# Kernel optimization log

Measured on AMD Instinct MI355X. Metric: run time of the kernel, lower is better.

The kernel has to match this reference:

```python
import jax, jax.numpy as jnp
import numpy as np

# Config constants (mirroring repo globals C.*)
B, L, D = 128, 200, 256          # batch, history length, d_model
NT = 10000                        # num_types (items)
NU = 50000                        # C.USER_NUMBER
NL = 4                            # n_layers
BETA_1 = 0.1                      # C.BETA_1


def _l2norm(x, eps):
    n = jnp.linalg.norm(x, axis=-1, keepdims=True)
    return x / jnp.maximum(n, eps)


def setup_inputs() -> dict:
    key = jax.random.key(0)
    ks = jax.random.split(key, 7)
    user_id = jax.random.randint(ks[0], (B,), 1, NU)
    event_type = jax.random.randint(ks[1], (B, L), 1, NT + 1)  # 1..NT (non-pad)
    adjacent_matrix = jax.random.uniform(ks[2], (NT, NT), jnp.float32)
    pop_encoding = jax.random.normal(ks[3], (NT + 1, D), jnp.float32) * 0.02
    event_emb_w = (jax.random.normal(ks[4], (NT + 1, D), jnp.float32) * 0.02).at[0].set(0.0)
    user_emb_w = (jax.random.normal(ks[5], (NU, D), jnp.float32) * 0.02).at[0].set(0.0)
    layer_ws = jax.random.normal(ks[6], (NL, D, D), jnp.float32) * 0.05
    return {"user_id": user_id, "event_type": event_type,
            "adjacent_matrix": adjacent_matrix, "pop_encoding": pop_encoding,
            "event_emb_w": event_emb_w, "user_emb_w": user_emb_w,
            "layer_ws": layer_ws}


def reference(user_id, event_type, adjacent_matrix, pop_encoding,
              event_emb_w, user_emb_w, layer_ws):
    # non-pad mask (pad idx = 0)
    non_pad = (event_type != 0).astype(jnp.float32)[..., None]  # (B,L,1)

    enc = event_emb_w[event_type]                 # (B,L,D)
    user = user_emb_w[user_id]                    # (B,D)
    pop = pop_encoding[event_type] * non_pad      # (B,L,D)

    # user-specific disentanglement: enc += sign(enc) * normalize(user)
    enc = enc + jnp.sign(enc) * _l2norm(user, 1e-12)[:, None, :]

    # batched adjacency gather: adj[b] = A[e-1][:, e-1] + A[e-1, e-1] (row-broadcast)
    idx = event_type - 1                          # (B,L)
    adj = adjacent_matrix[idx[:, :, None], idx[:, None, :]]      # (B,L,L)
    adj = adj + adjacent_matrix[idx, idx][:, None, :]            # diag broadcast over rows

    # hGCN layer stack: x <- leaky_relu((adj @ x) @ W)
    for i in range(NL):
        enc = jax.nn.leaky_relu(jnp.einsum('bls,bsd->bld', adj, enc) @ layer_ws[i])

    output = enc.mean(axis=1)                     # (B,D)
    user_embeddings = jnp.concatenate([output, pop.mean(axis=1) * BETA_1], axis=-1)  # (B,2D)

    # Predictor (evaluation=True path)
    item_encoding = event_emb_w[1:]               # (NT,D)
    out = user_embeddings[:, :D] @ item_encoding.T  # (B,NT)
    out = _l2norm(out, 1e-5)
    prediction = jnp.tanh(out)
    return prediction, user_embeddings, pop
```

## Files before the change

### kernel.cpp

```cpp
#include <hip/hip_runtime.h>
#include <math.h>

#define B_ 128
#define L_ 200
#define D_ 256
#define NT_ 10000
#define NL_ 4
#define BETA1 0.1f

typedef _Float16 f16x8 __attribute__((ext_vector_type(8)));
typedef _Float16 f16x4 __attribute__((ext_vector_type(4)));
typedef _Float16 f16x2 __attribute__((ext_vector_type(2)));
typedef float f32x4 __attribute__((ext_vector_type(4)));

__device__ __forceinline__ void split2(float v, _Float16& h, _Float16& l) {
    h = (_Float16)v;
    l = (_Float16)(v - (float)h);
}

struct HL { _Float16 h, l; };
__device__ __forceinline__ HL split2v(float v) {
    HL r;
    r.h = (_Float16)v;
    r.l = (_Float16)(v - (float)r.h);
    return r;
}

__device__ __forceinline__ float getscale(const unsigned int* amax, int i, int extra) {
    float am = fmaxf(__uint_as_float(amax[i]), 1e-30f);
    return scalbnf(1.f, 6 - ilogbf(am) - extra);
}

__global__ void init_kernel(float* __restrict__ ue, float* __restrict__ uePred,
                            unsigned int* __restrict__ amax) {
    int bid = blockIdx.x, tid = threadIdx.x;
    if (bid < 512) ue[bid * 256 + tid] = 0.f;
    else if (bid < 640) uePred[(bid - 512) * 256 + tid] = 0.f;
    else if (tid < 16) amax[tid] = 0u;
}

__global__ void user_norm_kernel(const int* __restrict__ user_id,
                                 const float* __restrict__ user_emb_w,
                                 float* __restrict__ unorm) {
    int b = blockIdx.x;
    int d = threadIdx.x;
    int uid = user_id[b];
    float v = user_emb_w[(long)uid * D_ + d];
    float sq = v * v;
    for (int off = 32; off > 0; off >>= 1) sq += __shfl_down(sq, off, 64);
    __shared__ float s[4];
    int wid = d >> 6, lane = d & 63;
    if (lane == 0) s[wid] = sq;
    __syncthreads();
    float n = sqrtf(s[0] + s[1] + s[2] + s[3]);
    n = fmaxf(n, 1e-12f);
    unorm[b * D_ + d] = v / n;
}

__global__ void enc0_kernel(const int* __restrict__ event_type,
                            const float* __restrict__ E,
                            const float* __restrict__ unorm,
                            float* __restrict__ encF,
                            unsigned int* __restrict__ amax) {
    int d = threadIdx.x;
    float m = 0.f;
    for (int bl = blockIdx.x; bl < B_ * L_; bl += gridDim.x) {
        int b = bl / L_;
        int et = event_type[bl];
        float e = E[(long)et * D_ + d];
        float sg = (e > 0.f) ? 1.f : ((e < 0.f) ? -1.f : 0.f);
        float u = unorm[b * D_ + d];
        float v = e + sg * u;
        encF[(long)bl * D_ + d] = v;
        m = fmaxf(m, fabsf(v));
    }
    for (int off = 32; off > 0; off >>= 1) m = fmaxf(m, __shfl_down(m, off, 64));
    __shared__ float sm[4];
    int wid = d >> 6, lane = d & 63;
    if (lane == 0) sm[wid] = m;
    __syncthreads();
    if (d == 0)
        atomicMax(amax, __float_as_uint(fmaxf(fmaxf(sm[0], sm[1]), fmaxf(sm[2], sm[3]))));
}

__global__ void pop_kernel(const int* __restrict__ event_type,
                           const float* __restrict__ pope,
                           float* __restrict__ pop_out) {
    int bl = blockIdx.x;
    int d = threadIdx.x;
    int et = event_type[bl];
    float np = (et != 0) ? 1.0f : 0.0f;
    pop_out[(long)bl * D_ + d] = pope[(long)et * D_ + d] * np;
}

__global__ void diag_kernel(const int* __restrict__ event_type,
                            const float* __restrict__ A,
                            float* __restrict__ diag) {
    int i = blockIdx.x * blockDim.x + threadIdx.x;
    if (i >= B_ * L_) return;
    long idx = (long)event_type[i] - 1;
    diag[i] = A[idx * NT_ + idx];
}

__global__ void adj_split_kernel(const int* __restrict__ event_type,
                                 const float* __restrict__ A,
                                 const float* __restrict__ diag,
                                 _Float16* __restrict__ adjH,
                                 _Float16* __restrict__ adjL) {
    int b = blockIdx.y;
    int i = blockIdx.x;
    int j = threadIdx.x;
    __shared__ int sidx[L_];
    __shared__ float sdiag[L_];
    if (j < L_) {
        sidx[j]  = event_type[b * L_ + j] - 1;
        sdiag[j] = diag[b * L_ + j];
    }
    __syncthreads();
    if (j >= L_) return;
    long row = (long)event_type[b * L_ + i] - 1;
    float v = A[row * NT_ + sidx[j]] + sdiag[j];
    long o = ((long)b * L_ + i) * L_ + j;
    _Float16 h, l;
    split2(v, h, l);
    adjH[o] = h; adjL[o] = l;
}

__global__ void wsplit_kernel(const float* __restrict__ W,
                              _Float16* __restrict__ WTh,
                              _Float16* __restrict__ WTl) {
    int layer = blockIdx.z;
    int k0 = blockIdx.y * 64, n0 = blockIdx.x * 64;
    const float* Wl = W + (long)layer * D_ * D_;
    __shared__ float t[64][65];
    int tid = threadIdx.x;
    for (int i = 0; i < 16; i++) {
        int idx = i * 256 + tid;
        int k = idx >> 6, n = idx & 63;
        t[k][n] = Wl[(long)(k0 + k) * D_ + n0 + n];
    }
    __syncthreads();
    for (int i = 0; i < 16; i++) {
        int idx = i * 256 + tid;
        int n = idx >> 6, k = idx & 63;
        float v = t[k][n];
        long o = (long)layer * D_ * D_ + (long)(n0 + n) * D_ + (k0 + k);
        _Float16 h, l;
        split2(v, h, l);
        WTh[o] = h; WTl[o] = l;
    }
}

__global__ void esplit_kernel(const float* __restrict__ E,
                              _Float16* __restrict__ ETh,
                              _Float16* __restrict__ ETl) {
    long f = ((long)blockIdx.x * 256 + threadIdx.x) * 4;
    float4 v = *(const float4*)(E + D_ + f);
    f16x4 h, l;
    HL r0 = split2v(v.x); h[0] = r0.h; l[0] = r0.l;
    HL r1 = split2v(v.y); h[1] = r1.h; l[1] = r1.l;
    HL r2 = split2v(v.z); h[2] = r2.h; l[2] = r2.l;
    HL r3 = split2v(v.w); h[3] = r3.h; l[3] = r3.l;
    *(f16x4*)(ETh + f) = h;
    *(f16x4*)(ETl + f) = l;
}

__global__ __launch_bounds__(256) void gemm1_kernel(
    const _Float16* __restrict__ adjH, const _Float16* __restrict__ adjL,
    const float* __restrict__ encF,
    _Float16* __restrict__ tmpH, _Float16* __restrict__ tmpL,
    const unsigned int* __restrict__ amax, int layer) {
    int b = blockIdx.z;
    const _Float16* Ah = adjH + (long)b * L_ * L_;
    const _Float16* Al = adjL + (long)b * L_ * L_;
    const float*    Bf = encF + (long)b * L_ * D_;
    int m0 = blockIdx.y * 128, n0 = blockIdx.x * 128;
    int tid = threadIdx.x, lane = tid & 63, wid = tid >> 6;
    int wr = wid >> 1, wc = wid & 1;
    float scale = getscale(amax, layer, 0);

    __shared__ _Float16 sAh[128][40], sAl[128][40];
    __shared__ _Float16 sBh[128][40], sBl[128][40];

    f32x4 acc[4][4] = {};
    int fr = lane & 15, kb = (lane >> 4) * 8, fq = lane >> 4;
    int nst = tid & 127, kkst = tid >> 7;

    for (int k0 = 0; k0 < L_; k0 += 32) {
#pragma unroll
        for (int c = 0; c < 2; c++) {
            int idx = c * 256 + tid;
            int row = idx >> 2, kq = (idx & 3) * 8;
            int gk = k0 + kq;
            f16x8 vh = {}, vl = {};
            if (m0 + row < L_ && gk < L_) {
                long o = (long)(m0 + row) * L_ + gk;
                vh = *(const f16x8*)(Ah + o);
                vl = *(const f16x8*)(Al + o);
            }
            *(f16x8*)&sAh[row][kq] = vh;
            *(f16x8*)&sAl[row][kq] = vl;
        }
#pragma unroll
        for (int it = 0; it < 8; it++) {
            int k = kkst * 16 + it * 2;
            int gk0 = k0 + k;
            float v0 = (gk0     < L_) ? Bf[(long)gk0 * D_ + n0 + nst] * scale : 0.f;
            float v1 = (gk0 + 1 < L_) ? Bf[(long)(gk0 + 1) * D_ + n0 + nst] * scale : 0.f;
            f16x2 h, l;
            HL r0 = split2v(v0); h[0] = r0.h; l[0] = r0.l;
            HL r1 = split2v(v1); h[1] = r1.h; l[1] = r1.l;
            int kx = k ^ ((nst & 3) << 3);
            *(f16x2*)&sBh[nst][kx] = h;
            *(f16x2*)&sBl[nst][kx] = l;
        }
        __syncthreads();

        f16x8 fbh[4], fbl[4];
#pragma unroll
        for (int n = 0; n < 4; n++) {
            int rB = wc * 64 + n * 16 + fr;
            int kbB = kb ^ ((rB & 3) << 3);
            fbh[n] = *(const f16x8*)&sBh[rB][kbB];
            fbl[n] = *(const f16x8*)&sBl[rB][kbB];
        }
#pragma unroll
        for (int m = 0; m < 4; m++) {
            int rA = wr * 64 + m * 16 + fr;
            f16x8 fah = *(const f16x8*)&sAh[rA][kb];
            f16x8 fal = *(const f16x8*)&sAl[rA][kb];
#pragma unroll
            for (int n = 0; n < 4; n++) {
                acc[m][n] = __builtin_amdgcn_mfma_f32_16x16x32_f16(fah, fbh[n], acc[m][n], 0, 0, 0);
                acc[m][n] = __builtin_amdgcn_mfma_f32_16x16x32_f16(fah, fbl[n], acc[m][n], 0, 0, 0);
                acc[m][n] = __builtin_amdgcn_mfma_f32_16x16x32_f16(fal, fbh[n], acc[m][n], 0, 0, 0);
            }
        }
        __syncthreads();
    }

    _Float16* Ch = tmpH + (long)b * L_ * D_;
    _Float16* Cl = tmpL + (long)b * L_ * D_;
#pragma unroll
    for (int m = 0; m < 4; m++)
#pragma unroll
        for (int n = 0; n < 4; n++)
#pragma unroll
            for (int r = 0; r < 4; r++) {
                int row = m0 + wr * 64 + m * 16 + fq * 4 + r;
                int col = n0 + wc * 64 + n * 16 + fr;
                if (row < L_) {
                    float v = acc[m][n][r];
                    _Float16 h, l;
                    split2(v, h, l);
                    long o = (long)row * D_ + col;
                    Ch[o] = h; Cl[o] = l;
                }
            }
}

__global__ __launch_bounds__(256) void gemm2_kernel(
    const _Float16* __restrict__ Ah, const _Float16* __restrict__ Al,
    const _Float16* __restrict__ Bh, const _Float16* __restrict__ Bl,
    float* __restrict__ Cf, unsigned int* __restrict__ amax) {
    int m0 = blockIdx.y * 128, n0 = blockIdx.x * 128;
    int tid = threadIdx.x, lane = tid & 63, wid = tid >> 6;
    int wr = wid >> 1, wc = wid & 1;
    __shared__ _Float16 sAh[128][40], sAl[128][40];
    __shared__ _Float16 sBh[128][40], sBl[128][40];
    __shared__ float sRed[4];
    f32x4 acc[4][4] = {};
    int fr = lane & 15, kb = (lane >> 4) * 8, fq = lane >> 4;

    for (int k0 = 0; k0 < D_; k0 += 32) {
#pragma unroll
        for (int c = 0; c < 2; c++) {
            int idx = c * 256 + tid;
            int row = idx >> 2, kq = (idx & 3) * 8, gk = k0 + kq;
            long oa = (long)(m0 + row) * D_ + gk;
            *(f16x8*)&sAh[row][kq] = *(const f16x8*)(Ah + oa);
            *(f16x8*)&sAl[row][kq] = *(const f16x8*)(Al + oa);
            long ob = (long)(n0 + row) * D_ + gk;
            *(f16x8*)&sBh[row][kq] = *(const f16x8*)(Bh + ob);
            *(f16x8*)&sBl[row][kq] = *(const f16x8*)(Bl + ob);
        }
        __syncthreads();
        f16x8 fbh[4], fbl[4];
#pragma unroll
        for (int n = 0; n < 4; n++) {
            int rB = wc * 64 + n * 16 + fr;
            fbh[n] = *(const f16x8*)&sBh[rB][kb];
            fbl[n] = *(const f16x8*)&sBl[rB][kb];
        }
#pragma unroll
        for (int m = 0; m < 4; m++) {
            int rA = wr * 64 + m * 16 + fr;
            f16x8 fah = *(const f16x8*)&sAh[rA][kb];
            f16x8 fal = *(const f16x8*)&sAl[rA][kb];
#pragma unroll
            for (int n = 0; n < 4; n++) {
                acc[m][n] = __builtin_amdgcn_mfma_f32_16x16x32_f16(fah, fbh[n], acc[m][n], 0, 0, 0);
                acc[m][n] = __builtin_amdgcn_mfma_f32_16x16x32_f16(fah, fbl[n], acc[m][n], 0, 0, 0);
                acc[m][n] = __builtin_amdgcn_mfma_f32_16x16x32_f16(fal, fbh[n], acc[m][n], 0, 0, 0);
            }
        }
        __syncthreads();
    }

    float tmax = 0.f;
#pragma unroll
    for (int m = 0; m < 4; m++)
#pragma unroll
        for (int n = 0; n < 4; n++)
#pragma unroll
            for (int r = 0; r < 4; r++) {
                int row = m0 + wr * 64 + m * 16 + fq * 4 + r;
                int col = n0 + wc * 64 + n * 16 + fr;
                float v = acc[m][n][r];
                v = (v >= 0.f) ? v : 0.01f * v;
                Cf[(long)row * D_ + col] = v;
                tmax = fmaxf(tmax, fabsf(v));
            }
    for (int off = 32; off > 0; off >>= 1) tmax = fmaxf(tmax, __shfl_down(tmax, off, 64));
    if (lane == 0) sRed[wid] = tmax;
    __syncthreads();
    if (tid == 0)
        atomicMax(amax, __float_as_uint(fmaxf(fmaxf(sRed[0], sRed[1]), fmaxf(sRed[2], sRed[3]))));
}

__global__ void mean_kernel(const float* __restrict__ encF,
                            const int* __restrict__ event_type,
                            const float* __restrict__ pope,
                            const unsigned int* __restrict__ amax,
                            float* __restrict__ ue,
                            float* __restrict__ uePred) {
    int b = blockIdx.x, chunk = blockIdx.y, d = threadIdx.x;
    float S = 1.f;
    for (int i = 0; i < NL_; i++) S *= getscale(amax, i, 0);
    float s1 = 0.f, s2 = 0.f;
    int l0 = chunk * 40;
    for (int l = l0; l < l0 + 40; l++) {
        s1 += encF[((long)b * L_ + l) * D_ + d];
        int et = event_type[b * L_ + l];
        s2 += (et != 0) ? pope[(long)et * D_ + d] : 0.f;
    }
    atomicAdd(&ue[b * 2 * D_ + d], s1 / (float)L_ / S);
    atomicAdd(&ue[b * 2 * D_ + D_ + d], s2 * (BETA1 / (float)L_));
    atomicAdd(&uePred[b * D_ + d], s1);
}

__global__ void uesplit_kernel(const float* __restrict__ uePred,
                               const unsigned int* __restrict__ amax,
                               _Float16* __restrict__ ueh,
                               _Float16* __restrict__ uel) {
    int b = blockIdx.x, d = threadIdx.x;
    float scale = getscale(amax, NL_, 8);
    float v = uePred[b * D_ + d] * scale;
    _Float16 h, l;
    split2(v, h, l);
    ueh[b * D_ + d] = h;
    uel[b * D_ + d] = l;
}

__global__ __launch_bounds__(256) void pred_mfma_kernel(
    const _Float16* __restrict__ Ah, const _Float16* __restrict__ Al,
    const _Float16* __restrict__ Bh, const _Float16* __restrict__ Bl,
    float* __restrict__ Cf) {
    int n0 = blockIdx.x * 64;
    int tid = threadIdx.x, lane = tid & 63, wid = tid >> 6;
    int wr = wid >> 1, wc = wid & 1;
    __shared__ _Float16 sAh[128][40], sAl[128][40];
    __shared__ _Float16 sBh[64][40], sBl[64][40];
    f32x4 acc[4][2] = {};
    int fr = lane & 15, kb = (lane >> 4) * 8, fq = lane >> 4;

    for (int k0 = 0; k0 < D_; k0 += 32) {
#pragma unroll
        for (int c = 0; c < 2; c++) {
            int idx = c * 256 + tid;
            int row = idx >> 2, kq = (idx & 3) * 8, gk = k0 + kq;
            long oa = (long)row * D_ + gk;
            *(f16x8*)&sAh[row][kq] = *(const f16x8*)(Ah + oa);
            *(f16x8*)&sAl[row][kq] = *(const f16x8*)(Al + oa);
        }
        {
            int row = tid >> 2, kq = (tid & 3) * 8, gk = k0 + kq;
            f16x8 wh = {}, wl = {};
            if (n0 + row < NT_) {
                long ob = (long)(n0 + row) * D_ + gk;
                wh = *(const f16x8*)(Bh + ob);
                wl = *(const f16x8*)(Bl + ob);
            }
            *(f16x8*)&sBh[row][kq] = wh;
            *(f16x8*)&sBl[row][kq] = wl;
        }
        __syncthreads();
        f16x8 fbh[2], fbl[2];
#pragma unroll
        for (int n = 0; n < 2; n++) {
            int rB = wc * 32 + n * 16 + fr;
            fbh[n] = *(const f16x8*)&sBh[rB][kb];
            fbl[n] = *(const f16x8*)&sBl[rB][kb];
        }
#pragma unroll
        for (int m = 0; m < 4; m++) {
            int rA = wr * 64 + m * 16 + fr;
            f16x8 fah = *(const f16x8*)&sAh[rA][kb];
            f16x8 fal = *(const f16x8*)&sAl[rA][kb];
#pragma unroll
            for (int n = 0; n < 2; n++) {
                acc[m][n] = __builtin_amdgcn_mfma_f32_16x16x32_f16(fah, fbh[n], acc[m][n], 0, 0, 0);
                acc[m][n] = __builtin_amdgcn_mfma_f32_16x16x32_f16(fah, fbl[n], acc[m][n], 0, 0, 0);
                acc[m][n] = __builtin_amdgcn_mfma_f32_16x16x32_f16(fal, fbh[n], acc[m][n], 0, 0, 0);
            }
        }
        __syncthreads();
    }
#pragma unroll
    for (int m = 0; m < 4; m++)
#pragma unroll
        for (int n = 0; n < 2; n++)
#pragma unroll
            for (int r = 0; r < 4; r++) {
                int row = wr * 64 + m * 16 + fq * 4 + r;
                int col = n0 + wc * 32 + n * 16 + fr;
                if (col < NT_)
                    Cf[(long)row * NT_ + col] = acc[m][n][r];
            }
}

__global__ void norms_kernel(const float* __restrict__ pred, float* __restrict__ norms) {
    int b = blockIdx.x, t = threadIdx.x;
    const float* row = pred + (long)b * NT_;
    float sq = 0.f;
    for (int i = t; i < NT_; i += 1024) { float v = row[i]; sq += v * v; }
    for (int off = 32; off > 0; off >>= 1) sq += __shfl_down(sq, off, 64);
    __shared__ float s[16];
    if ((t & 63) == 0) s[t >> 6] = sq;
    __syncthreads();
    if (t == 0) {
        float n = 0.f;
        for (int i = 0; i < 16; i++) n += s[i];
        norms[b] = 1.f / fmaxf(sqrtf(n), 1e-5f);
    }
}

__global__ void tanh_apply_kernel(float* __restrict__ pred, const float* __restrict__ norms) {
    int b = blockIdx.x, chunk = blockIdx.y, t = threadIdx.x;
    float inv = norms[b];
    float* row = pred + (long)b * NT_;
    int start = chunk * 2000;
    for (int i = start + t; i < start + 2000; i += 256)
        row[i] = tanhf(row[i] * inv);
}

template <bool BT, bool LEAKY>
__global__ void gemm_kernel(const float* __restrict__ A,
                            const float* __restrict__ Bm,
                            float* __restrict__ C,
                            int M, int N, int K, int lda, int ldb, int ldc,
                            long strideA, long strideB, long strideC) {
    int batch = blockIdx.z;
    A  += (long)batch * strideA;
    Bm += (long)batch * strideB;
    C  += (long)batch * strideC;
    const int BM = 64, BN = 64, BK = 16;
    __shared__ float As[BK][BM + 1];
    __shared__ float Bs[BK][BN + 1];
    int tid = threadIdx.x;
    int m0 = blockIdx.y * BM, n0 = blockIdx.x * BN;
    int tx = tid & 15, ty = tid >> 4;
    float acc[4][4] = {};
    for (int k0 = 0; k0 < K; k0 += BK) {
        {
            int m = tid >> 2, kk = (tid & 3) * 4;
            int gm = m0 + m;
#pragma unroll
            for (int q = 0; q < 4; q++) {
                int gk = k0 + kk + q;
                float x = (gm < M && gk < K) ? A[(long)gm * lda + gk] : 0.f;
                As[kk + q][m] = x;
            }
        }
        if (!BT) {
            int kk = tid >> 4, n = (tid & 15) * 4;
            int gk = k0 + kk;
#pragma unroll
            for (int q = 0; q < 4; q++) {
                int gn = n0 + n + q;
                float x = (gk < K && gn < N) ? Bm[(long)gk * ldb + gn] : 0.f;
                Bs[kk][n + q] = x;
            }
        } else {
            int n = tid >> 2, kk = (tid & 3) * 4;
            int gn = n0 + n;
#pragma unroll
            for (int q = 0; q < 4; q++) {
                int gk = k0 + kk + q;
                float x = (gn < N && gk < K) ? Bm[(long)gn * ldb + gk] : 0.f;
                Bs[kk + q][n] = x;
            }
        }
        __syncthreads();
#pragma unroll
        for (int kk = 0; kk < BK; kk++) {
            float a[4], bv[4];
#pragma unroll
            for (int q = 0; q < 4; q++) a[q] = As[kk][ty * 4 + q];
#pragma unroll
            for (int q = 0; q < 4; q++) bv[q] = Bs[kk][tx * 4 + q];
#pragma unroll
            for (int i = 0; i < 4; i++)
#pragma unroll
                for (int j = 0; j < 4; j++)
                    acc[i][j] += a[i] * bv[j];
        }
        __syncthreads();
    }
#pragma unroll
    for (int i = 0; i < 4; i++) {
        int gm = m0 + ty * 4 + i;
        if (gm >= M) continue;
#pragma unroll
        for (int j = 0; j < 4; j++) {
            int gn = n0 + tx * 4 + j;
            if (gn >= N) continue;
            float v = acc[i][j];
            if (LEAKY) v = (v >= 0.f) ? v : 0.01f * v;
            C[(long)gm * ldc + gn] = v;
        }
    }
}

__global__ void mean_plain_kernel(const float* __restrict__ enc,
                                  const int* __restrict__ event_type,
                                  const float* __restrict__ pope,
                                  float* __restrict__ ue) {
    int b = blockIdx.x, d = threadIdx.x;
    float s1 = 0.f, s2 = 0.f;
    for (int l = 0; l < L_; l++) {
        s1 += enc[((long)b * L_ + l) * D_ + d];
        int et = event_type[b * L_ + l];
        float np = (et != 0) ? 1.0f : 0.0f;
        s2 += pope[(long)et * D_ + d] * np;
    }
    ue[b * (2 * D_) + d]      = s1 / (float)L_;
    ue[b * (2 * D_) + D_ + d] = (s2 / (float)L_) * BETA1;
}

__global__ void adj_kernel_f32(const int* __restrict__ event_type,
                               const float* __restrict__ A,
                               const float* __restrict__ diag,
                               float* __restrict__ adj) {
    int b = blockIdx.y;
    int i = blockIdx.x;
    int j = threadIdx.x;
    __shared__ int sidx[L_];
    __shared__ float sdiag[L_];
    if (j < L_) {
        sidx[j]  = event_type[b * L_ + j] - 1;
        sdiag[j] = diag[b * L_ + j];
    }
    __syncthreads();
    if (j >= L_) return;
    long row = (long)event_type[b * L_ + i] - 1;
    adj[((long)b * L_ + i) * L_ + j] = A[row * NT_ + sidx[j]] + sdiag[j];
}

__global__ void normtanh_kernel(float* __restrict__ pred) {
    int b = blockIdx.x;
    int t = threadIdx.x;
    float* row = pred + (long)b * NT_;
    float sq = 0.f;
    for (int i = t; i < NT_; i += 256) { float v = row[i]; sq += v * v; }
    for (int off = 32; off > 0; off >>= 1) sq += __shfl_down(sq, off, 64);
    __shared__ float s[4];
    int wid = t >> 6, lane = t & 63;
    if (lane == 0) s[wid] = sq;
    __syncthreads();
    float n = sqrtf(s[0] + s[1] + s[2] + s[3]);
    n = fmaxf(n, 1e-5f);
    float inv = 1.f / n;
    for (int i = t; i < NT_; i += 256) row[i] = tanhf(row[i] * inv);
}

extern "C" void kernel_launch(void* const* d_in, const int* in_sizes, int n_in,
                              void* d_out, int out_size, void* d_ws, size_t ws_size,
                              hipStream_t stream) {
    const int*   user_id    = (const int*)d_in[0];
    const int*   event_type = (const int*)d_in[1];
    const float* A          = (const float*)d_in[2];
    const float* pope       = (const float*)d_in[3];
    const float* E          = (const float*)d_in[4];
    const float* U          = (const float*)d_in[5];
    const float* W          = (const float*)d_in[6];

    float* out  = (float*)d_out;
    float* pred = out;
    float* ue   = out + (long)B_ * NT_;
    float* pop  = ue  + (long)B_ * 2 * D_;

    char* w = (char*)d_ws;
    auto carve = [&](size_t bytes) { char* p = w; w += (bytes + 255) & ~(size_t)255; return p; };
    unsigned int* amax = (unsigned int*)carve(64);
    _Float16* adjH   = (_Float16*)carve((size_t)B_ * L_ * L_ * 2);
    _Float16* adjL   = (_Float16*)carve((size_t)B_ * L_ * L_ * 2);
    _Float16* tmpH   = (_Float16*)carve((size_t)B_ * L_ * D_ * 2);
    _Float16* tmpL   = (_Float16*)carve((size_t)B_ * L_ * D_ * 2);
    float*    encF   = (float*)carve((size_t)B_ * L_ * D_ * 4);
    _Float16* WTh    = (_Float16*)carve((size_t)NL_ * D_ * D_ * 2);
    _Float16* WTl    = (_Float16*)carve((size_t)NL_ * D_ * D_ * 2);
    _Float16* ETh    = (_Float16*)carve((size_t)NT_ * D_ * 2);
    _Float16* ETl    = (_Float16*)carve((size_t)NT_ * D_ * 2);
    float*    uePred = (float*)carve((size_t)B_ * D_ * 4);
    _Float16* ueh    = (_Float16*)carve((size_t)B_ * D_ * 2);
    _Float16* uel    = (_Float16*)carve((size_t)B_ * D_ * 2);
    float*    unorm  = (float*)carve((size_t)B_ * D_ * 4);
    float*    diag   = (float*)carve((size_t)B_ * L_ * 4);
    float*    norms  = (float*)carve((size_t)B_ * 4);
    size_t needed = (size_t)(w - (char*)d_ws);

    if (ws_size >= needed) {
        init_kernel<<<641, 256, 0, stream>>>(ue, uePred, amax);
        user_norm_kernel<<<B_, 256, 0, stream>>>(user_id, U, unorm);
        enc0_kernel<<<1280, 256, 0, stream>>>(event_type, E, unorm, encF, amax);
        pop_kernel<<<B_ * L_, 256, 0, stream>>>(event_type, pope, pop);
        diag_kernel<<<(B_ * L_ + 255) / 256, 256, 0, stream>>>(event_type, A, diag);
        adj_split_kernel<<<dim3(L_, B_), 256, 0, stream>>>(event_type, A, diag, adjH, adjL);
        wsplit_kernel<<<dim3(4, 4, NL_), 256, 0, stream>>>(W, WTh, WTl);
        esplit_kernel<<<NT_ * D_ / 1024, 256, 0, stream>>>(E, ETh, ETl);

        for (int i = 0; i < NL_; i++) {
            gemm1_kernel<<<dim3(2, 2, B_), 256, 0, stream>>>(
                adjH, adjL, encF, tmpH, tmpL, amax, i);
            gemm2_kernel<<<dim3(2, B_ * L_ / 128), 256, 0, stream>>>(
                tmpH, tmpL, WTh + (long)i * D_ * D_, WTl + (long)i * D_ * D_,
                encF, amax + i + 1);
        }

        mean_kernel<<<dim3(B_, 5), 256, 0, stream>>>(encF, event_type, pope, amax, ue, uePred);
        uesplit_kernel<<<B_, 256, 0, stream>>>(uePred, amax, ueh, uel);
        pred_mfma_kernel<<<(NT_ + 63) / 64, 256, 0, stream>>>(ueh, uel, ETh, ETl, pred);
        norms_kernel<<<B_, 1024, 0, stream>>>(pred, norms);
        tanh_apply_kernel<<<dim3(B_, 5), 256, 0, stream>>>(pred, norms);
    } else {
        float* ws0   = (float*)d_ws;
        float* uno   = ws0;
        float* dia   = uno + B_ * D_;
        float* adjF  = dia + B_ * L_;
        float* encA  = adjF + (long)B_ * L_ * L_;
        float* encB  = encA + (long)B_ * L_ * D_;
        float* tmp   = pop;

        user_norm_kernel<<<B_, 256, 0, stream>>>(user_id, U, uno);
        enc0_kernel<<<1280, 256, 0, stream>>>(event_type, E, uno, encA, (unsigned int*)dia);
        diag_kernel<<<(B_ * L_ + 255) / 256, 256, 0, stream>>>(event_type, A, dia);
        adj_kernel_f32<<<dim3(L_, B_), 256, 0, stream>>>(event_type, A, dia, adjF);

        float* cur = encA; float* nxt = encB;
        for (int i = 0; i < NL_; i++) {
            dim3 g1((D_ + 63) / 64, (L_ + 63) / 64, B_);
            gemm_kernel<false, false><<<g1, 256, 0, stream>>>(
                adjF, cur, tmp, L_, D_, L_, L_, D_, D_,
                (long)L_ * L_, (long)L_ * D_, (long)L_ * D_);
            dim3 g2((D_ + 63) / 64, (B_ * L_ + 63) / 64, 1);
            gemm_kernel<false, true><<<g2, 256, 0, stream>>>(
                tmp, W + (long)i * D_ * D_, nxt, B_ * L_, D_, D_, D_, D_, D_, 0, 0, 0);
            float* t = cur; cur = nxt; nxt = t;
        }
        pop_kernel<<<B_ * L_, 256, 0, stream>>>(event_type, pope, pop);
        mean_plain_kernel<<<B_, 256, 0, stream>>>(cur, event_type, pope, ue);

        dim3 g3((NT_ + 63) / 64, (B_ + 63) / 64, 1);
        gemm_kernel<true, false><<<g3, 256, 0, stream>>>(
            ue, E + D_, pred, B_, NT_, D_, 2 * D_, D_, NT_, 0, 0, 0);
        normtanh_kernel<<<B_, 256, 0, stream>>>(pred);
    }
}
```

Measured before the change: 432.5 us.

## Fuse per-layer GEMM pair, merge enc/pop, mean/split and norm/tanh kernels

Each layer now runs one kernel that computes adj@enc into registers, splits the result to fp16 hi/lo pairs in shared memory, and multiplies it by W in place. This removes the intermediate tmp buffer and one launch per layer. Also merges pop into enc0, mean with uesplit (removing atomics and the init of ue/uePred), and norms with tanh, and batches 25 rows per block in the adjacency gather. In exchange, the fused layer kernel has only 256 blocks of 512 threads and large shared memory, which lowers occupancy. It also reads W fragments straight from global memory.

```diff
diff --git a/kernel.cpp b/kernel.cpp
--- a/kernel.cpp
+++ b/kernel.cpp
@@ -31,12 +31,8 @@
     return scalbnf(1.f, 6 - ilogbf(am) - extra);
 }
 
-__global__ void init_kernel(float* __restrict__ ue, float* __restrict__ uePred,
-                            unsigned int* __restrict__ amax) {
-    int bid = blockIdx.x, tid = threadIdx.x;
-    if (bid < 512) ue[bid * 256 + tid] = 0.f;
-    else if (bid < 640) uePred[(bid - 512) * 256 + tid] = 0.f;
-    else if (tid < 16) amax[tid] = 0u;
+__global__ void init_amax_kernel(unsigned int* __restrict__ amax) {
+    if (threadIdx.x < 16) amax[threadIdx.x] = 0u;
 }
 
 __global__ void user_norm_kernel(const int* __restrict__ user_id,
@@ -57,11 +53,13 @@
     unorm[b * D_ + d] = v / n;
 }
 
-__global__ void enc0_kernel(const int* __restrict__ event_type,
-                            const float* __restrict__ E,
-                            const float* __restrict__ unorm,
-                            float* __restrict__ encF,
-                            unsigned int* __restrict__ amax) {
+__global__ void enc0pop_kernel(const int* __restrict__ event_type,
+                               const float* __restrict__ E,
+                               const float* __restrict__ pope,
+                               const float* __restrict__ unorm,
+                               float* __restrict__ encF,
+                               float* __restrict__ pop_out,
+                               unsigned int* __restrict__ amax) {
     int d = threadIdx.x;
     float m = 0.f;
     for (int bl = blockIdx.x; bl < B_ * L_; bl += gridDim.x) {
@@ -73,6 +71,7 @@
         float v = e + sg * u;
         encF[(long)bl * D_ + d] = v;
         m = fmaxf(m, fabsf(v));
+        pop_out[(long)bl * D_ + d] = (et != 0) ? pope[(long)et * D_ + d] : 0.f;
     }
     for (int off = 32; off > 0; off >>= 1) m = fmaxf(m, __shfl_down(m, off, 64));
     __shared__ float sm[4];
@@ -81,16 +80,6 @@
     __syncthreads();
     if (d == 0)
         atomicMax(amax, __float_as_uint(fmaxf(fmaxf(sm[0], sm[1]), fmaxf(sm[2], sm[3]))));
-}
-
-__global__ void pop_kernel(const int* __restrict__ event_type,
-                           const float* __restrict__ pope,
-                           float* __restrict__ pop_out) {
-    int bl = blockIdx.x;
-    int d = threadIdx.x;
-    int et = event_type[bl];
-    float np = (et != 0) ? 1.0f : 0.0f;
-    pop_out[(long)bl * D_ + d] = pope[(long)et * D_ + d] * np;
 }
 
 __global__ void diag_kernel(const int* __restrict__ event_type,
@@ -102,13 +91,13 @@
     diag[i] = A[idx * NT_ + idx];
 }
 
-__global__ void adj_split_kernel(const int* __restrict__ event_type,
-                                 const float* __restrict__ A,
-                                 const float* __restrict__ diag,
-                                 _Float16* __restrict__ adjH,
-                                 _Float16* __restrict__ adjL) {
+__global__ void adj_split2_kernel(const int* __restrict__ event_type,
+                                  const float* __restrict__ A,
+                                  const float* __restrict__ diag,
+                                  _Float16* __restrict__ adjH,
+                                  _Float16* __restrict__ adjL) {
     int b = blockIdx.y;
-    int i = blockIdx.x;
+    int chunk = blockIdx.x;
     int j = threadIdx.x;
     __shared__ int sidx[L_];
     __shared__ float sdiag[L_];
@@ -118,12 +107,15 @@
     }
     __syncthreads();
     if (j >= L_) return;
-    long row = (long)event_type[b * L_ + i] - 1;
-    float v = A[row * NT_ + sidx[j]] + sdiag[j];
-    long o = ((long)b * L_ + i) * L_ + j;
-    _Float16 h, l;
-    split2(v, h, l);
-    adjH[o] = h; adjL[o] = l;
+    int i0 = chunk * 25;
+#pragma unroll 5
+    for (int i = i0; i < i0 + 25; i++) {
+        long rowi = (long)sidx[i];
+        float v = A[rowi * NT_ + sidx[j]] + sdiag[j];
+        HL r = split2v(v);
+        long o = ((long)b * L_ + i) * L_ + j;
+        adjH[o] = r.h; adjL[o] = r.l;
+    }
 }
 
 __global__ void wsplit_kernel(const float* __restrict__ W,
@@ -165,33 +157,37 @@
     *(f16x4*)(ETl + f) = l;
 }
 
-__global__ __launch_bounds__(256) void gemm1_kernel(
-    const _Float16* __restrict__ adjH, const _Float16* __restrict__ adjL,
-    const float* __restrict__ encF,
-    _Float16* __restrict__ tmpH, _Float16* __restrict__ tmpL,
-    const unsigned int* __restrict__ amax, int layer) {
-    int b = blockIdx.z;
-    const _Float16* Ah = adjH + (long)b * L_ * L_;
-    const _Float16* Al = adjL + (long)b * L_ * L_;
-    const float*    Bf = encF + (long)b * L_ * D_;
-    int m0 = blockIdx.y * 128, n0 = blockIdx.x * 128;
+__global__ __launch_bounds__(512) void layer_fused_kernel(
+    const _Float16* __restrict__ adjHg, const _Float16* __restrict__ adjLg,
+    const float* __restrict__ encIn,
+    const _Float16* __restrict__ WThg, const _Float16* __restrict__ WTlg,
+    float* __restrict__ encOut,
+    const unsigned int* __restrict__ amaxIn, unsigned int* __restrict__ amaxOut) {
+    int b = blockIdx.y;
+    int m0 = blockIdx.x * 128;
+    const _Float16* Ah = adjHg + (long)b * L_ * L_;
+    const _Float16* Al = adjLg + (long)b * L_ * L_;
+    const float*    Bf = encIn + (long)b * L_ * D_;
     int tid = threadIdx.x, lane = tid & 63, wid = tid >> 6;
-    int wr = wid >> 1, wc = wid & 1;
-    float scale = getscale(amax, layer, 0);
-
-    __shared__ _Float16 sAh[128][40], sAl[128][40];
-    __shared__ _Float16 sBh[128][40], sBl[128][40];
-
-    f32x4 acc[4][4] = {};
-    int fr = lane & 15, kb = (lane >> 4) * 8, fq = lane >> 4;
-    int nst = tid & 127, kkst = tid >> 7;
+    int wr = wid >> 2, wc = wid & 3;
+    int fr = lane & 15, fq = lane >> 4, kb = fq * 8;
+    float scale = getscale(amaxIn, 0, 0);
+
+    __shared__ char smem[61440];
+    __shared__ float sRed[8];
+    _Float16 (*sAh)[40] = (_Float16(*)[40])(smem);
+    _Float16 (*sAl)[40] = (_Float16(*)[40])(smem + 10240);
+    _Float16 (*sBh)[40] = (_Float16(*)[40])(smem + 20480);
+    _Float16 (*sBl)[40] = (_Float16(*)[40])(smem + 40960);
+    _Float16 (*tH)[80]  = (_Float16(*)[80])(smem + 20480);
+    _Float16 (*tL)[80]  = (_Float16(*)[80])(smem + 40960);
+
+    f32x4 acc1[4][4] = {};
+    int nst = tid & 255, kst = tid >> 8;
 
     for (int k0 = 0; k0 < L_; k0 += 32) {
-#pragma unroll
-        for (int c = 0; c < 2; c++) {
-            int idx = c * 256 + tid;
-            int row = idx >> 2, kq = (idx & 3) * 8;
-            int gk = k0 + kq;
+        {
+            int row = tid >> 2, kq = (tid & 3) * 8, gk = k0 + kq;
             f16x8 vh = {}, vl = {};
             if (m0 + row < L_ && gk < L_) {
                 long o = (long)(m0 + row) * L_ + gk;
@@ -203,10 +199,10 @@
         }
 #pragma unroll
         for (int it = 0; it < 8; it++) {
-            int k = kkst * 16 + it * 2;
+            int k = kst * 16 + it * 2;
             int gk0 = k0 + k;
-            float v0 = (gk0     < L_) ? Bf[(long)gk0 * D_ + n0 + nst] * scale : 0.f;
-            float v1 = (gk0 + 1 < L_) ? Bf[(long)(gk0 + 1) * D_ + n0 + nst] * scale : 0.f;
+            float v0 = (gk0     < L_) ? Bf[(long)gk0 * D_ + nst] * scale : 0.f;
+            float v1 = (gk0 + 1 < L_) ? Bf[(long)(gk0 + 1) * D_ + nst] * scale : 0.f;
             f16x2 h, l;
             HL r0 = split2v(v0); h[0] = r0.h; l[0] = r0.l;
             HL r1 = split2v(v1); h[1] = r1.h; l[1] = r1.l;
@@ -220,9 +216,9 @@
 #pragma unroll
         for (int n = 0; n < 4; n++) {
             int rB = wc * 64 + n * 16 + fr;
-            int kbB = kb ^ ((rB & 3) << 3);
-            fbh[n] = *(const f16x8*)&sBh[rB][kbB];
-            fbl[n] = *(const f16x8*)&sBl[rB][kbB];
+            int kx = kb ^ ((rB & 3) << 3);
+            fbh[n] = *(const f16x8*)&sBh[rB][kx];
+            fbl[n] = *(const f16x8*)&sBl[rB][kx];
         }
 #pragma unroll
         for (int m = 0; m < 4; m++) {
@@ -231,16 +227,61 @@
             f16x8 fal = *(const f16x8*)&sAl[rA][kb];
 #pragma unroll
             for (int n = 0; n < 4; n++) {
-                acc[m][n] = __builtin_amdgcn_mfma_f32_16x16x32_f16(fah, fbh[n], acc[m][n], 0, 0, 0);
-                acc[m][n] = __builtin_amdgcn_mfma_f32_16x16x32_f16(fah, fbl[n], acc[m][n], 0, 0, 0);
-                acc[m][n] = __builtin_amdgcn_mfma_f32_16x16x32_f16(fal, fbh[n], acc[m][n], 0, 0, 0);
-            }
-        }
-        __syncthreads();
-    }
-
-    _Float16* Ch = tmpH + (long)b * L_ * D_;
-    _Float16* Cl = tmpL + (long)b * L_ * D_;
+                acc1[m][n] = __builtin_amdgcn_mfma_f32_16x16x32_f16(fah, fbh[n], acc1[m][n], 0, 0, 0);
+                acc1[m][n] = __builtin_amdgcn_mfma_f32_16x16x32_f16(fah, fbl[n], acc1[m][n], 0, 0, 0);
+                acc1[m][n] = __builtin_amdgcn_mfma_f32_16x16x32_f16(fal, fbh[n], acc1[m][n], 0, 0, 0);
+            }
+        }
+        __syncthreads();
+    }
+
+    f32x4 acc2[4][4] = {};
+    for (int q = 0; q < 4; q++) {
+        if (wc == q) {
+#pragma unroll
+            for (int m = 0; m < 4; m++)
+#pragma unroll
+                for (int n = 0; n < 4; n++)
+#pragma unroll
+                    for (int r = 0; r < 4; r++) {
+                        int row = wr * 64 + m * 16 + fq * 4 + r;
+                        int col = n * 16 + fr;
+                        int cx = col ^ (((row >> 2) & 3) << 3);
+                        HL s = split2v(acc1[m][n][r]);
+                        tH[row][cx] = s.h;
+                        tL[row][cx] = s.l;
+                    }
+        }
+        __syncthreads();
+#pragma unroll
+        for (int ks = 0; ks < 2; ks++) {
+            int gk = q * 64 + ks * 32 + kb;
+            f16x8 fbh[4], fbl[4];
+#pragma unroll
+            for (int n = 0; n < 4; n++) {
+                long o = (long)(wc * 64 + n * 16 + fr) * D_ + gk;
+                fbh[n] = *(const f16x8*)(WThg + o);
+                fbl[n] = *(const f16x8*)(WTlg + o);
+            }
+#pragma unroll
+            for (int m = 0; m < 4; m++) {
+                int rA = wr * 64 + m * 16 + fr;
+                int kx = (ks * 32 + kb) ^ (((rA >> 2) & 3) << 3);
+                f16x8 fah = *(const f16x8*)&tH[rA][kx];
+                f16x8 fal = *(const f16x8*)&tL[rA][kx];
+#pragma unroll
+                for (int n = 0; n < 4; n++) {
+                    acc2[m][n] = __builtin_amdgcn_mfma_f32_16x16x32_f16(fah, fbh[n], acc2[m][n], 0, 0, 0);
+                    acc2[m][n] = __builtin_amdgcn_mfma_f32_16x16x32_f16(fah, fbl[n], acc2[m][n], 0, 0, 0);
+                    acc2[m][n] = __builtin_amdgcn_mfma_f32_16x16x32_f16(fal, fbh[n], acc2[m][n], 0, 0, 0);
+                }
+            }
+        }
+        __syncthreads();
+    }
+
+    float* Cf = encOut + (long)b * L_ * D_;
+    float tmax = 0.f;
 #pragma unroll
     for (int m = 0; m < 4; m++)
 #pragma unroll
@@ -248,118 +289,46 @@
 #pragma unroll
             for (int r = 0; r < 4; r++) {
                 int row = m0 + wr * 64 + m * 16 + fq * 4 + r;
-                int col = n0 + wc * 64 + n * 16 + fr;
+                int col = wc * 64 + n * 16 + fr;
                 if (row < L_) {
-                    float v = acc[m][n][r];
-                    _Float16 h, l;
-                    split2(v, h, l);
-                    long o = (long)row * D_ + col;
-                    Ch[o] = h; Cl[o] = l;
+                    float v = acc2[m][n][r];
+                    v = (v >= 0.f) ? v : 0.01f * v;
+                    Cf[(long)row * D_ + col] = v;
+                    tmax = fmaxf(tmax, fabsf(v));
                 }
-            }
-}
-
-__global__ __launch_bounds__(256) void gemm2_kernel(
-    const _Float16* __restrict__ Ah, const _Float16* __restrict__ Al,
-    const _Float16* __restrict__ Bh, const _Float16* __restrict__ Bl,
-    float* __restrict__ Cf, unsigned int* __restrict__ amax) {
-    int m0 = blockIdx.y * 128, n0 = blockIdx.x * 128;
-    int tid = threadIdx.x, lane = tid & 63, wid = tid >> 6;
-    int wr = wid >> 1, wc = wid & 1;
-    __shared__ _Float16 sAh[128][40], sAl[128][40];
-    __shared__ _Float16 sBh[128][40], sBl[128][40];
-    __shared__ float sRed[4];
-    f32x4 acc[4][4] = {};
-    int fr = lane & 15, kb = (lane >> 4) * 8, fq = lane >> 4;
-
-    for (int k0 = 0; k0 < D_; k0 += 32) {
-#pragma unroll
-        for (int c = 0; c < 2; c++) {
-            int idx = c * 256 + tid;
-            int row = idx >> 2, kq = (idx & 3) * 8, gk = k0 + kq;
-            long oa = (long)(m0 + row) * D_ + gk;
-            *(f16x8*)&sAh[row][kq] = *(const f16x8*)(Ah + oa);
-            *(f16x8*)&sAl[row][kq] = *(const f16x8*)(Al + oa);
-            long ob = (long)(n0 + row) * D_ + gk;
-            *(f16x8*)&sBh[row][kq] = *(const f16x8*)(Bh + ob);
-            *(f16x8*)&sBl[row][kq] = *(const f16x8*)(Bl + ob);
-        }
-        __syncthreads();
-        f16x8 fbh[4], fbl[4];
-#pragma unroll
-        for (int n = 0; n < 4; n++) {
-            int rB = wc * 64 + n * 16 + fr;
-            fbh[n] = *(const f16x8*)&sBh[rB][kb];
-            fbl[n] = *(const f16x8*)&sBl[rB][kb];
-        }
-#pragma unroll
-        for (int m = 0; m < 4; m++) {
-            int rA = wr * 64 + m * 16 + fr;
-            f16x8 fah = *(const f16x8*)&sAh[rA][kb];
-            f16x8 fal = *(const f16x8*)&sAl[rA][kb];
-#pragma unroll
-            for (int n = 0; n < 4; n++) {
-                acc[m][n] = __builtin_amdgcn_mfma_f32_16x16x32_f16(fah, fbh[n], acc[m][n], 0, 0, 0);
-                acc[m][n] = __builtin_amdgcn_mfma_f32_16x16x32_f16(fah, fbl[n], acc[m][n], 0, 0, 0);
-                acc[m][n] = __builtin_amdgcn_mfma_f32_16x16x32_f16(fal, fbh[n], acc[m][n], 0, 0, 0);
-            }
-        }
-        __syncthreads();
-    }
-
-    float tmax = 0.f;
-#pragma unroll
-    for (int m = 0; m < 4; m++)
-#pragma unroll
-        for (int n = 0; n < 4; n++)
-#pragma unroll
-            for (int r = 0; r < 4; r++) {
-                int row = m0 + wr * 64 + m * 16 + fq * 4 + r;
-                int col = n0 + wc * 64 + n * 16 + fr;
-                float v = acc[m][n][r];
-                v = (v >= 0.f) ? v : 0.01f * v;
-                Cf[(long)row * D_ + col] = v;
-                tmax = fmaxf(tmax, fabsf(v));
             }
     for (int off = 32; off > 0; off >>= 1) tmax = fmaxf(tmax, __shfl_down(tmax, off, 64));
     if (lane == 0) sRed[wid] = tmax;
     __syncthreads();
-    if (tid == 0)
-        atomicMax(amax, __float_as_uint(fmaxf(fmaxf(sRed[0], sRed[1]), fmaxf(sRed[2], sRed[3]))));
-}
-
-__global__ void mean_kernel(const float* __restrict__ encF,
-                            const int* __restrict__ event_type,
-                            const float* __restrict__ pope,
-                            const unsigned int* __restrict__ amax,
-                            float* __restrict__ ue,
-                            float* __restrict__ uePred) {
-    int b = blockIdx.x, chunk = blockIdx.y, d = threadIdx.x;
+    if (tid == 0) {
+        float v = 0.f;
+        for (int i = 0; i < 8; i++) v = fmaxf(v, sRed[i]);
+        atomicMax(amaxOut, __float_as_uint(v));
+    }
+}
+
+__global__ void mean_fused_kernel(const float* __restrict__ encF,
+                                  const int* __restrict__ event_type,
+                                  const float* __restrict__ pope,
+                                  const unsigned int* __restrict__ amax,
+                                  float* __restrict__ ue,
+                                  _Float16* __restrict__ ueh,
+                                  _Float16* __restrict__ uel) {
+    int b = blockIdx.x, d = threadIdx.x;
     float S = 1.f;
     for (int i = 0; i < NL_; i++) S *= getscale(amax, i, 0);
     float s1 = 0.f, s2 = 0.f;
-    int l0 = chunk * 40;
-    for (int l = l0; l < l0 + 40; l++) {
+    for (int l = 0; l < L_; l++) {
         s1 += encF[((long)b * L_ + l) * D_ + d];
         int et = event_type[b * L_ + l];
         s2 += (et != 0) ? pope[(long)et * D_ + d] : 0.f;
     }
-    atomicAdd(&ue[b * 2 * D_ + d], s1 / (float)L_ / S);
-    atomicAdd(&ue[b * 2 * D_ + D_ + d], s2 * (BETA1 / (float)L_));
-    atomicAdd(&uePred[b * D_ + d], s1);
-}
-
-__global__ void uesplit_kernel(const float* __restrict__ uePred,
-                               const unsigned int* __restrict__ amax,
-                               _Float16* __restrict__ ueh,
-                               _Float16* __restrict__ uel) {
-    int b = blockIdx.x, d = threadIdx.x;
-    float scale = getscale(amax, NL_, 8);
-    float v = uePred[b * D_ + d] * scale;
-    _Float16 h, l;
-    split2(v, h, l);
-    ueh[b * D_ + d] = h;
-    uel[b * D_ + d] = l;
+    ue[b * 2 * D_ + d]      = s1 / (float)L_ / S;
+    ue[b * 2 * D_ + D_ + d] = s2 * (BETA1 / (float)L_);
+    float sc = getscale(amax, NL_, 8);
+    HL r = split2v(s1 * sc);
+    ueh[b * D_ + d] = r.h;
+    uel[b * D_ + d] = r.l;
 }
 
 __global__ __launch_bounds__(256) void pred_mfma_kernel(
@@ -429,29 +398,54 @@
             }
 }
 
-__global__ void norms_kernel(const float* __restrict__ pred, float* __restrict__ norms) {
+__global__ void normtanh2_kernel(float* __restrict__ pred) {
     int b = blockIdx.x, t = threadIdx.x;
-    const float* row = pred + (long)b * NT_;
+    float* row = pred + (long)b * NT_;
+    float v[10];
     float sq = 0.f;
-    for (int i = t; i < NT_; i += 1024) { float v = row[i]; sq += v * v; }
+#pragma unroll
+    for (int p = 0; p < 10; p++) {
+        int i = p * 1024 + t;
+        v[p] = (i < NT_) ? row[i] : 0.f;
+        sq += v[p] * v[p];
+    }
     for (int off = 32; off > 0; off >>= 1) sq += __shfl_down(sq, off, 64);
     __shared__ float s[16];
     if ((t & 63) == 0) s[t >> 6] = sq;
     __syncthreads();
-    if (t == 0) {
-        float n = 0.f;
-        for (int i = 0; i < 16; i++) n += s[i];
-        norms[b] = 1.f / fmaxf(sqrtf(n), 1e-5f);
-    }
-}
-
-__global__ void tanh_apply_kernel(float* __restrict__ pred, const float* __restrict__ norms) {
-    int b = blockIdx.x, chunk = blockIdx.y, t = threadIdx.x;
-    float inv = norms[b];
-    float* row = pred + (long)b * NT_;
-    int start = chunk * 2000;
-    for (int i = start + t; i < start + 2000; i += 256)
-        row[i] = tanhf(row[i] * inv);
+    float n = 0.f;
+    for (int i = 0; i < 16; i++) n += s[i];
+    float inv = 1.f / fmaxf(sqrtf(n), 1e-5f);
+#pragma unroll
+    for (int p = 0; p < 10; p++) {
+        int i = p * 1024 + t;
+        if (i < NT_) row[i] = tanhf(v[p] * inv);
+    }
+}
+
+__global__ void enc0_kernel(const int* __restrict__ event_type,
+                            const float* __restrict__ E,
+                            const float* __restrict__ unorm,
+                            float* __restrict__ encF) {
+    int d = threadIdx.x;
+    for (int bl = blockIdx.x; bl < B_ * L_; bl += gridDim.x) {
+        int b = bl / L_;
+        int et = event_type[bl];
+        float e = E[(long)et * D_ + d];
+        float sg = (e > 0.f) ? 1.f : ((e < 0.f) ? -1.f : 0.f);
+        float u = unorm[b * D_ + d];
+        encF[(long)bl * D_ + d] = e + sg * u;
+    }
+}
+
+__global__ void pop_kernel(const int* __restrict__ event_type,
+                           const float* __restrict__ pope,
+                           float* __restrict__ pop_out) {
+    int bl = blockIdx.x;
+    int d = threadIdx.x;
+    int et = event_type[bl];
+    float np = (et != 0) ? 1.0f : 0.0f;
+    pop_out[(long)bl * D_ + d] = pope[(long)et * D_ + d] * np;
 }
 
 template <bool BT, bool LEAKY>
@@ -603,61 +597,56 @@
     char* w = (char*)d_ws;
     auto carve = [&](size_t bytes) { char* p = w; w += (bytes + 255) & ~(size_t)255; return p; };
     unsigned int* amax = (unsigned int*)carve(64);
-    _Float16* adjH   = (_Float16*)carve((size_t)B_ * L_ * L_ * 2);
-    _Float16* adjL   = (_Float16*)carve((size_t)B_ * L_ * L_ * 2);
-    _Float16* tmpH   = (_Float16*)carve((size_t)B_ * L_ * D_ * 2);
-    _Float16* tmpL   = (_Float16*)carve((size_t)B_ * L_ * D_ * 2);
-    float*    encF   = (float*)carve((size_t)B_ * L_ * D_ * 4);
-    _Float16* WTh    = (_Float16*)carve((size_t)NL_ * D_ * D_ * 2);
-    _Float16* WTl    = (_Float16*)carve((size_t)NL_ * D_ * D_ * 2);
-    _Float16* ETh    = (_Float16*)carve((size_t)NT_ * D_ * 2);
-    _Float16* ETl    = (_Float16*)carve((size_t)NT_ * D_ * 2);
-    float*    uePred = (float*)carve((size_t)B_ * D_ * 4);
-    _Float16* ueh    = (_Float16*)carve((size_t)B_ * D_ * 2);
-    _Float16* uel    = (_Float16*)carve((size_t)B_ * D_ * 2);
-    float*    unorm  = (float*)carve((size_t)B_ * D_ * 4);
-    float*    diag   = (float*)carve((size_t)B_ * L_ * 4);
-    float*    norms  = (float*)carve((size_t)B_ * 4);
+    _Float16* adjH  = (_Float16*)carve((size_t)B_ * L_ * L_ * 2);
+    _Float16* adjL  = (_Float16*)carve((size_t)B_ * L_ * L_ * 2);
+    float*    encA  = (float*)carve((size_t)B_ * L_ * D_ * 4);
+    float*    encB  = (float*)carve((size_t)B_ * L_ * D_ * 4);
+    _Float16* WTh   = (_Float16*)carve((size_t)NL_ * D_ * D_ * 2);
+    _Float16* WTl   = (_Float16*)carve((size_t)NL_ * D_ * D_ * 2);
+    _Float16* ETh   = (_Float16*)carve((size_t)NT_ * D_ * 2);
+    _Float16* ETl   = (_Float16*)carve((size_t)NT_ * D_ * 2);
+    _Float16* ueh   = (_Float16*)carve((size_t)B_ * D_ * 2);
+    _Float16* uel   = (_Float16*)carve((size_t)B_ * D_ * 2);
+    float*    unorm = (float*)carve((size_t)B_ * D_ * 4);
+    float*    diag  = (float*)carve((size_t)B_ * L_ * 4);
     size_t needed = (size_t)(w - (char*)d_ws);
 
     if (ws_size >= needed) {
-        init_kernel<<<641, 256, 0, stream>>>(ue, uePred, amax);
+        init_amax_kernel<<<1, 64, 0, stream>>>(amax);
         user_norm_kernel<<<B_, 256, 0, stream>>>(user_id, U, unorm);
-        enc0_kernel<<<1280, 256, 0, stream>>>(event_type, E, unorm, encF, amax);
-        pop_kernel<<<B_ * L_, 256, 0, stream>>>(event_type, pope, pop);
+        enc0pop_kernel<<<1280, 256, 0, stream>>>(event_type, E, pope, unorm, encA, pop, amax);
         diag_kernel<<<(B_ * L_ + 255) / 256, 256, 0, stream>>>(event_type, A, diag);
-        adj_split_kernel<<<dim3(L_, B_), 256, 0, stream>>>(event_type, A, diag, adjH, adjL);
+        adj_split2_kernel<<<dim3(8, B_), 256, 0, stream>>>(event_type, A, diag, adjH, adjL);
         wsplit_kernel<<<dim3(4, 4, NL_), 256, 0, stream>>>(W, WTh, WTl);
         esplit_kernel<<<NT_ * D_ / 1024, 256, 0, stream>>>(E, ETh, ETl);
 
+        float* cur = encA; float* nxt = encB;
         for (int i = 0; i < NL_; i++) {
-            gemm1_kernel<<<dim3(2, 2, B_), 256, 0, stream>>>(
-                adjH, adjL, encF, tmpH, tmpL, amax, i);
-            gemm2_kernel<<<dim3(2, B_ * L_ / 128), 256, 0, stream>>>(
-                tmpH, tmpL, WTh + (long)i * D_ * D_, WTl + (long)i * D_ * D_,
-                encF, amax + i + 1);
-        }
-
-        mean_kernel<<<dim3(B_, 5), 256, 0, stream>>>(encF, event_type, pope, amax, ue, uePred);
-        uesplit_kernel<<<B_, 256, 0, stream>>>(uePred, amax, ueh, uel);
+            layer_fused_kernel<<<dim3(2, B_), 512, 0, stream>>>(
+                adjH, adjL, cur,
+                WTh + (long)i * D_ * D_, WTl + (long)i * D_ * D_,
+                nxt, amax + i, amax + i + 1);
+            float* t = cur; cur = nxt; nxt = t;
+        }
+
+        mean_fused_kernel<<<B_, 256, 0, stream>>>(cur, event_type, pope, amax, ue, ueh, uel);
         pred_mfma_kernel<<<(NT_ + 63) / 64, 256, 0, stream>>>(ueh, uel, ETh, ETl, pred);
-        norms_kernel<<<B_, 1024, 0, stream>>>(pred, norms);
-        tanh_apply_kernel<<<dim3(B_, 5), 256, 0, stream>>>(pred, norms);
+        normtanh2_kernel<<<B_, 1024, 0, stream>>>(pred);
     } else {
         float* ws0   = (float*)d_ws;
         float* uno   = ws0;
         float* dia   = uno + B_ * D_;
         float* adjF  = dia + B_ * L_;
-        float* encA  = adjF + (long)B_ * L_ * L_;
-        float* encB  = encA + (long)B_ * L_ * D_;
+        float* encA2 = adjF + (long)B_ * L_ * L_;
+        float* encB2 = encA2 + (long)B_ * L_ * D_;
         float* tmp   = pop;
 
         user_norm_kernel<<<B_, 256, 0, stream>>>(user_id, U, uno);
-        enc0_kernel<<<1280, 256, 0, stream>>>(event_type, E, uno, encA, (unsigned int*)dia);
+        enc0_kernel<<<1280, 256, 0, stream>>>(event_type, E, uno, encA2);
         diag_kernel<<<(B_ * L_ + 255) / 256, 256, 0, stream>>>(event_type, A, dia);
         adj_kernel_f32<<<dim3(L_, B_), 256, 0, stream>>>(event_type, A, dia, adjF);
 
-        float* cur = encA; float* nxt = encB;
+        float* cur = encA2; float* nxt = encB2;
         for (int i = 0; i < NL_; i++) {
             dim3 g1((D_ + 63) / 64, (L_ + 63) / 64, B_);
             gemm_kernel<false, false><<<g1, 256, 0, stream>>>(
```

Measured after the change: 454.4 us. 1.05x slower.
